# Kernel optimization log

Measured on AMD Instinct MI355X. Metric: run time of the kernel, lower is better.

Reference implementation:

```python
import jax, jax.numpy as jnp
import numpy as np

D_MODEL = 2048
N_HEADS = 16
D_HEAD = D_MODEL // N_HEADS


def setup_inputs() -> dict:
    key = jax.random.key(0)
    ks = jax.random.split(key, 8)
    B, T = 2, 2048
    s = 1.0 / np.sqrt(D_MODEL)
    return {
        "q": jax.random.normal(ks[0], (B, T, D_MODEL), jnp.float32),
        "k": jax.random.normal(ks[1], (B, T, D_MODEL), jnp.float32),
        "v": jax.random.normal(ks[2], (B, T, D_MODEL), jnp.float32),
        "Wq": jax.random.normal(ks[3], (D_MODEL, D_MODEL), jnp.float32) * s,
        "Wk": jax.random.normal(ks[4], (D_MODEL, D_MODEL), jnp.float32) * s,
        "Wv": jax.random.normal(ks[5], (D_MODEL, D_MODEL), jnp.float32) * s,
        "Wo": jax.random.normal(ks[6], (D_MODEL, D_MODEL), jnp.float32) * s,
        "bo": jax.random.normal(ks[7], (D_MODEL,), jnp.float32) * 0.01,
    }


def reference(q, k, v, Wq, Wk, Wv, Wo, bo):
    B, T, C = q.shape
    scale = D_HEAD ** -0.5
    # projections (torch Linear: x @ W.T), split into heads: [B, H, T, Dh]
    qh = (q @ Wq.T).reshape(B, T, N_HEADS, D_HEAD).transpose(0, 2, 1, 3)
    kh = (k @ Wk.T).reshape(B, -1, N_HEADS, D_HEAD).transpose(0, 2, 1, 3)
    vh = (v @ Wv.T).reshape(B, -1, N_HEADS, D_HEAD).transpose(0, 2, 1, 3)
    scores = jnp.einsum("bhqd,bhkd->bhqk", qh, kh) * scale  # [B,H,T,T]
    attn = jax.nn.softmax(scores, axis=-1)
    out = jnp.einsum("bhqk,bhkd->bhqd", attn, vh)  # [B,H,T,Dh]
    out = out.transpose(0, 2, 1, 3).reshape(B, T, C)
    return out @ Wo.T + bo
```

## Files before the change

### kernel.cpp

```cpp
#include <hip/hip_runtime.h>
#include <hip/hip_bf16.h>

typedef unsigned int u32;
typedef unsigned long long u64;
typedef unsigned short u16;
typedef __bf16 bf16_t;
typedef bf16_t bf16x8 __attribute__((ext_vector_type(8)));
typedef float f32x4 __attribute__((ext_vector_type(4)));
typedef float f32x4v __attribute__((ext_vector_type(4)));
typedef u16 u16x8 __attribute__((ext_vector_type(8)));

#define GLB __attribute__((address_space(1)))
#define LDSAS __attribute__((address_space(3)))

#define DM 2048
#define NH 16
#define DH 128
#define BB 2
#define TT 2048
#define MT (BB*TT)

static __device__ __forceinline__ u16 f2bf(float f){
    u32 x = __builtin_bit_cast(u32, f);
    return (u16)((x + 0x7FFFu + ((x >> 16) & 1u)) >> 16);
}

static __device__ __forceinline__ f32x4 mfma16(bf16x8 a, bf16x8 b, f32x4 c){
    return __builtin_amdgcn_mfma_f32_16x16x32_bf16(a, b, c, 0, 0, 0);
}

static __device__ __forceinline__ void gload_lds16(const u16* g, u16* l){
    __builtin_amdgcn_global_load_lds((const GLB u32*)g, (LDSAS u32*)l, 16, 0, 0);
}

__global__ __launch_bounds__(256) void cast_all(
    const float* __restrict__ q, const float* __restrict__ kin, const float* __restrict__ v,
    const float* __restrict__ wq, const float* __restrict__ wk, const float* __restrict__ wv,
    const float* __restrict__ wo,
    u16* __restrict__ qb, u16* __restrict__ kb, u16* __restrict__ vb,
    u16* __restrict__ wqb, u16* __restrict__ wkb, u16* __restrict__ wvb, u16* __restrict__ wob)
{
    const int QC = MT*DM/8;
    const int WC = DM*DM/8;
    int idx = blockIdx.x*256 + threadIdx.x;
    const float* src; u16* dst; int off;
    if (idx < 3*QC){
        int w = idx / QC; off = idx - w*QC;
        src = (w==0) ? q : (w==1) ? kin : v;
        dst = (w==0) ? qb : (w==1) ? kb : vb;
    } else {
        int j = idx - 3*QC; int w = j / WC; off = j - w*WC;
        src = (w==0) ? wq : (w==1) ? wk : (w==2) ? wv : wo;
        dst = (w==0) ? wqb : (w==1) ? wkb : (w==2) ? wvb : wob;
    }
    const f32x4v* s4 = (const f32x4v*)(src + (u64)off*8);
    f32x4v a = s4[0], b = s4[1];
    u16x8 r;
    r[0]=f2bf(a[0]); r[1]=f2bf(a[1]); r[2]=f2bf(a[2]); r[3]=f2bf(a[3]);
    r[4]=f2bf(b[0]); r[5]=f2bf(b[1]); r[6]=f2bf(b[2]); r[7]=f2bf(b[3]);
    *(u16x8*)(dst + (u64)off*8) = r;
}

template<int MODE>
__global__ __launch_bounds__(256) void gemm_bt(
    const u16* __restrict__ A0, const u16* __restrict__ B0, void* __restrict__ C0,
    const u16* __restrict__ A1, const u16* __restrict__ B1, void* __restrict__ C1,
    const u16* __restrict__ A2, const u16* __restrict__ B2, void* __restrict__ C2,
    const float* __restrict__ bias)
{
    __shared__ u16 Ash[128*32];
    __shared__ u16 Bsh[128*32];
    const u16 *A, *B; void* C;
    {
        int z = blockIdx.z;
        A = (z==0)?A0:(z==1)?A1:A2;
        B = (z==0)?B0:(z==1)?B1:B2;
        C = (z==0)?C0:(z==1)?C1:C2;
    }
    const int tid = threadIdx.x;
    const int lane = tid & 63;
    const int wave = tid >> 6;
    const int wr = wave >> 1, wc = wave & 1;
    const int g = lane >> 4, r16 = lane & 15;
    const int bm = blockIdx.y, bn = blockIdx.x;

    int srow[2], scol[2];
    #pragma unroll
    for (int rd = 0; rd < 2; rd++){
        int i = rd*256 + tid;
        int row = i >> 2;
        int c = (i & 3) ^ ((row >> 1) & 3);
        srow[rd] = row; scol[rd] = c*8;
    }
    const u16* Ag = A + (u64)(bm*128)*DM;
    const u16* Bg = B + (u64)(bn*128)*DM;

    int aoff[4], boff[4];
    #pragma unroll
    for (int mi = 0; mi < 4; mi++){
        int row = wr*64 + mi*16 + r16;
        int c = g ^ ((row >> 1) & 3);
        aoff[mi] = row*32 + c*8;
    }
    #pragma unroll
    for (int ni = 0; ni < 4; ni++){
        int row = wc*64 + ni*16 + r16;
        int c = g ^ ((row >> 1) & 3);
        boff[ni] = row*32 + c*8;
    }

    f32x4 acc[4][4] = {};

    for (int k0 = 0; k0 < DM; k0 += 32){
        #pragma unroll
        for (int rd = 0; rd < 2; rd++){
            int i = rd*256 + tid;
            gload_lds16(Ag + (u64)srow[rd]*DM + k0 + scol[rd], Ash + i*8);
            gload_lds16(Bg + (u64)srow[rd]*DM + k0 + scol[rd], Bsh + i*8);
        }
        __syncthreads();
        bf16x8 af[4], bfr[4];
        #pragma unroll
        for (int mi = 0; mi < 4; mi++) af[mi] = *(const bf16x8*)(Ash + aoff[mi]);
        #pragma unroll
        for (int ni = 0; ni < 4; ni++) bfr[ni] = *(const bf16x8*)(Bsh + boff[ni]);
        #pragma unroll
        for (int mi = 0; mi < 4; mi++)
            #pragma unroll
            for (int ni = 0; ni < 4; ni++)
                acc[mi][ni] = mfma16(af[mi], bfr[ni], acc[mi][ni]);
        __syncthreads();
    }

    #pragma unroll
    for (int mi = 0; mi < 4; mi++){
        #pragma unroll
        for (int ni = 0; ni < 4; ni++){
            int row0 = bm*128 + wr*64 + mi*16 + 4*g;
            int col  = bn*128 + wc*64 + ni*16 + r16;
            if (MODE == 0){
                u16* Cp = (u16*)C;
                #pragma unroll
                for (int rr = 0; rr < 4; rr++)
                    Cp[(u64)(row0+rr)*DM + col] = f2bf(acc[mi][ni][rr]);
            } else {
                float* Cp = (float*)C;
                float bv = bias[col];
                #pragma unroll
                for (int rr = 0; rr < 4; rr++)
                    Cp[(u64)(row0+rr)*DM + col] = acc[mi][ni][rr] + bv;
            }
        }
    }
}

__global__ __launch_bounds__(256) void transpose_v(
    const u16* __restrict__ Vh, u16* __restrict__ Vt)
{
    __shared__ u16 tile[64*80];
    int t0 = blockIdx.x*64, d0 = blockIdx.y*64, bh = blockIdx.z;
    int b = bh >> 4, h = bh & 15;
    int tid = threadIdx.x;
    #pragma unroll
    for (int rd = 0; rd < 2; rd++){
        int i = rd*256 + tid;
        int row = i >> 3, c = i & 7;
        u16x8 vv = *(const u16x8*)(Vh + (u64)(b*TT + t0 + row)*DM + h*DH + d0 + c*8);
        *(u16x8*)(tile + row*80 + c*8) = vv;
    }
    __syncthreads();
    #pragma unroll
    for (int rd = 0; rd < 2; rd++){
        int i = rd*256 + tid;
        int d = i >> 3, tc = (i & 7)*8;
        u16x8 vv;
        #pragma unroll
        for (int j = 0; j < 8; j++) vv[j] = tile[(tc + j)*80 + d];
        *(u16x8*)(Vt + (u64)(bh*DH + d0 + d)*TT + t0 + tc) = vv;
    }
}

__global__ __launch_bounds__(256) void flash_attn(
    const u16* __restrict__ Qh, const u16* __restrict__ Kh,
    const u16* __restrict__ Vt, u16* __restrict__ Ao)
{
    __shared__ u16 Ksh[64*128];
    __shared__ u16 Vsh[128*64];
    __shared__ u16 Psh[4*16*64];
    const int qt = blockIdx.x, h = blockIdx.y, b = blockIdx.z;
    const int tid = threadIdx.x, lane = tid & 63, wave = tid >> 6;
    const int g = lane >> 4, r16 = lane & 15;
    const int bh = b*NH + h;

    bf16x8 qf[4];
    {
        const u16* qp = Qh + (u64)(b*TT + qt*64 + wave*16 + r16)*DM + h*DH + g*8;
        #pragma unroll
        for (int kc = 0; kc < 4; kc++) qf[kc] = *(const bf16x8*)(qp + kc*32);
    }
    f32x4 accO[8] = {};
    float mrow[4], lrow[4];
    #pragma unroll
    for (int r = 0; r < 4; r++){ mrow[r] = -1e30f; lrow[r] = 0.f; }
    const float scale = 0.08838834764831845f;

    u16* Pw = Psh + wave*16*64;

    for (int kv0 = 0; kv0 < TT; kv0 += 64){
        #pragma unroll
        for (int rd = 0; rd < 4; rd++){
            int i = rd*256 + tid;
            int row = i >> 4, c = (i & 15) ^ (row & 7);
            gload_lds16(Kh + (u64)(b*TT + kv0 + row)*DM + h*DH + c*8, Ksh + i*8);
        }
        #pragma unroll
        for (int rd = 0; rd < 4; rd++){
            int i = rd*256 + tid;
            int row = i >> 3, c = (i & 7) ^ (row & 7);
            gload_lds16(Vt + (u64)(bh*DH + row)*TT + kv0 + c*8, Vsh + i*8);
        }
        __syncthreads();

        f32x4 s[4];
        #pragma unroll
        for (int nf = 0; nf < 4; nf++){
            f32x4 a = {0.f, 0.f, 0.f, 0.f};
            #pragma unroll
            for (int kc = 0; kc < 4; kc++){
                int row = nf*16 + r16;
                int c = (kc*4 + g) ^ (r16 & 7);
                bf16x8 kfr = *(const bf16x8*)(Ksh + row*128 + c*8);
                a = mfma16(qf[kc], kfr, a);
            }
            s[nf] = a * scale;
        }
        #pragma unroll
        for (int r = 0; r < 4; r++){
            float mx = fmaxf(fmaxf(s[0][r], s[1][r]), fmaxf(s[2][r], s[3][r]));
            #pragma unroll
            for (int d = 1; d < 16; d <<= 1) mx = fmaxf(mx, __shfl_xor(mx, d));
            float mnew = fmaxf(mrow[r], mx);
            float alpha = __expf(mrow[r] - mnew);
            mrow[r] = mnew;
            float ls = 0.f;
            #pragma unroll
            for (int nf = 0; nf < 4; nf++){
                float p = __expf(s[nf][r] - mnew);
                s[nf][r] = p;
                ls += p;
            }
            #pragma unroll
            for (int d = 1; d < 16; d <<= 1) ls += __shfl_xor(ls, d);
            lrow[r] = lrow[r]*alpha + ls;
            #pragma unroll
            for (int nfd = 0; nfd < 8; nfd++) accO[nfd][r] *= alpha;
        }
        #pragma unroll
        for (int r = 0; r < 4; r++){
            int qrow = 4*g + r;
            #pragma unroll
            for (int nf = 0; nf < 4; nf++){
                int kv = nf*16 + r16;
                int c = (kv >> 3) ^ (qrow & 7);
                Pw[qrow*64 + c*8 + (kv & 7)] = f2bf(s[nf][r]);
            }
        }
        #pragma unroll
        for (int kvc = 0; kvc < 2; kvc++){
            int cpa = (kvc*4 + g) ^ (r16 & 7);
            bf16x8 pa = *(const bf16x8*)(Pw + r16*64 + cpa*8);
            #pragma unroll
            for (int nfd = 0; nfd < 8; nfd++){
                int rowv = nfd*16 + r16;
                int cv = (kvc*4 + g) ^ (r16 & 7);
                bf16x8 vfr = *(const bf16x8*)(Vsh + rowv*64 + cv*8);
                accO[nfd] = mfma16(pa, vfr, accO[nfd]);
            }
        }
        __syncthreads();
    }

    #pragma unroll
    for (int nfd = 0; nfd < 8; nfd++){
        #pragma unroll
        for (int r = 0; r < 4; r++){
            int row = b*TT + qt*64 + wave*16 + 4*g + r;
            int col = h*DH + nfd*16 + r16;
            float o = accO[nfd][r] / lrow[r];
            Ao[(u64)row*DM + col] = f2bf(o);
        }
    }
}

extern "C" void kernel_launch(void* const* d_in, const int* in_sizes, int n_in,
                              void* d_out, int out_size, void* d_ws, size_t ws_size,
                              hipStream_t stream)
{
    const float* q  = (const float*)d_in[0];
    const float* k  = (const float*)d_in[1];
    const float* v  = (const float*)d_in[2];
    const float* wq = (const float*)d_in[3];
    const float* wk = (const float*)d_in[4];
    const float* wv = (const float*)d_in[5];
    const float* wo = (const float*)d_in[6];
    const float* bo = (const float*)d_in[7];
    float* out = (float*)d_out;

    const u64 SZQ = (u64)MT*DM;
    const u64 SZW = (u64)DM*DM;
    u16* ws  = (u16*)d_ws;
    u16* qb  = ws;
    u16* kb  = ws + SZQ;
    u16* vb  = ws + 2*SZQ;
    u16* wqb = ws + 3*SZQ;
    u16* wkb = wqb + SZW;
    u16* wvb = wqb + 2*SZW;
    u16* wob = wqb + 3*SZW;
    u16* qh  = ws + 5*SZQ;
    u16* kh  = ws + 6*SZQ;
    u16* vh  = ws + 7*SZQ;
    u16* vt  = qb;
    u16* ao  = vb;

    cast_all<<<dim3(20480), dim3(256), 0, stream>>>(
        q, k, v, wq, wk, wv, wo, qb, kb, vb, wqb, wkb, wvb, wob);

    gemm_bt<0><<<dim3(16, 32, 3), dim3(256), 0, stream>>>(
        qb, wqb, qh, kb, wkb, kh, vb, wvb, vh, nullptr);

    transpose_v<<<dim3(32, 2, 32), dim3(256), 0, stream>>>(vh, vt);

    flash_attn<<<dim3(32, 16, 2), dim3(256), 0, stream>>>(qh, kh, vt, ao);

    gemm_bt<1><<<dim3(16, 32, 1), dim3(256), 0, stream>>>(
        ao, wob, (void*)out, ao, wob, (void*)out, ao, wob, (void*)out, bo);
}
```

Baseline: 536.4 us.

## Rewrite flash attention with 32x32 MFMA, transposed S, double-buffered KV, register P

Replaces the flash attention kernel with a 512-thread, 256-query-row block that computes S transposed using 32x32x16 bf16 MFMA. Each lane then owns one query row, so softmax needs only a single cross-half shuffle. P is packed to bf16 in registers with v_cvt_pk and permlane32_swap instead of going through LDS. K/V tiles are double-buffered so the next tile's loads overlap compute, and blocks are remapped so heads sharing a query tile run close together. The aim is fewer LDS round trips and reductions and higher MFMA density, at the cost of more registers and inline asm that depends on the gfx950 ISA.

```diff
diff --git a/kernel.cpp b/kernel.cpp
--- a/kernel.cpp
+++ b/kernel.cpp
@@ -7,8 +7,10 @@
 typedef __bf16 bf16_t;
 typedef bf16_t bf16x8 __attribute__((ext_vector_type(8)));
 typedef float f32x4 __attribute__((ext_vector_type(4)));
+typedef float f32x16 __attribute__((ext_vector_type(16)));
 typedef float f32x4v __attribute__((ext_vector_type(4)));
 typedef u16 u16x8 __attribute__((ext_vector_type(8)));
+typedef u32 u32x4 __attribute__((ext_vector_type(4)));
 
 #define GLB __attribute__((address_space(1)))
 #define LDSAS __attribute__((address_space(3)))
@@ -27,6 +29,14 @@
 
 static __device__ __forceinline__ f32x4 mfma16(bf16x8 a, bf16x8 b, f32x4 c){
     return __builtin_amdgcn_mfma_f32_16x16x32_bf16(a, b, c, 0, 0, 0);
+}
+
+static __device__ __forceinline__ f32x16 mfma32(bf16x8 a, bf16x8 b, f32x16 c){
+    return __builtin_amdgcn_mfma_f32_32x32x16_bf16(a, b, c, 0, 0, 0);
+}
+
+static __device__ __forceinline__ u32 cvtpk(float lo, float hi){
+    u32 r; asm("v_cvt_pk_bf16_f32 %0, %1, %2" : "=v"(r) : "v"(lo), "v"(hi)); return r;
 }
 
 static __device__ __forceinline__ void gload_lds16(const u16* g, u16* l){
@@ -180,114 +190,137 @@
     }
 }
 
-__global__ __launch_bounds__(256) void flash_attn(
+static __device__ __forceinline__ void stage_kv(
+    const u16* __restrict__ Kbase, const u16* __restrict__ Vbase,
+    u16* ksh, u16* vsh, int tid)
+{
+    #pragma unroll
+    for (int rd = 0; rd < 2; rd++){
+        int ci = rd*512 + tid;
+        int row = ci >> 4, ch = (ci & 15) ^ (row & 7);
+        gload_lds16(Kbase + (u64)row*DM + ch*8, ksh + ci*8);
+    }
+    #pragma unroll
+    for (int rd = 0; rd < 2; rd++){
+        int ci = rd*512 + tid;
+        int row = ci >> 3, ch = (ci & 7) ^ (row & 7);
+        gload_lds16(Vbase + (u64)row*TT + ch*8, vsh + ci*8);
+    }
+}
+
+__global__ __launch_bounds__(512, 2) void flash_attn2(
     const u16* __restrict__ Qh, const u16* __restrict__ Kh,
     const u16* __restrict__ Vt, u16* __restrict__ Ao)
 {
-    __shared__ u16 Ksh[64*128];
-    __shared__ u16 Vsh[128*64];
-    __shared__ u16 Psh[4*16*64];
-    const int qt = blockIdx.x, h = blockIdx.y, b = blockIdx.z;
+    __shared__ __align__(16) u16 Ksh[2][64*128];
+    __shared__ __align__(16) u16 Vsh[2][128*64];
+    __shared__ __align__(16) float asc[8][32];
+
+    const int f = blockIdx.x + 8*(blockIdx.y + 16*blockIdx.z);
+    const int qt = f >> 5, bhl = f & 31;
+    const int b = bhl >> 4, h = bhl & 15;
+    const int bh = b*NH + h;
+
     const int tid = threadIdx.x, lane = tid & 63, wave = tid >> 6;
-    const int g = lane >> 4, r16 = lane & 15;
-    const int bh = b*NH + h;
-
-    bf16x8 qf[4];
+    const int l31 = lane & 31, hi = lane >> 5, l7 = lane & 7;
+    const float scale = 0.08838834764831845f;
+
+    bf16x8 qf[8];
     {
-        const u16* qp = Qh + (u64)(b*TT + qt*64 + wave*16 + r16)*DM + h*DH + g*8;
-        #pragma unroll
-        for (int kc = 0; kc < 4; kc++) qf[kc] = *(const bf16x8*)(qp + kc*32);
-    }
-    f32x4 accO[8] = {};
-    float mrow[4], lrow[4];
-    #pragma unroll
-    for (int r = 0; r < 4; r++){ mrow[r] = -1e30f; lrow[r] = 0.f; }
-    const float scale = 0.08838834764831845f;
-
-    u16* Pw = Psh + wave*16*64;
-
-    for (int kv0 = 0; kv0 < TT; kv0 += 64){
-        #pragma unroll
-        for (int rd = 0; rd < 4; rd++){
-            int i = rd*256 + tid;
-            int row = i >> 4, c = (i & 15) ^ (row & 7);
-            gload_lds16(Kh + (u64)(b*TT + kv0 + row)*DM + h*DH + c*8, Ksh + i*8);
-        }
-        #pragma unroll
-        for (int rd = 0; rd < 4; rd++){
-            int i = rd*256 + tid;
-            int row = i >> 3, c = (i & 7) ^ (row & 7);
-            gload_lds16(Vt + (u64)(bh*DH + row)*TT + kv0 + c*8, Vsh + i*8);
+        const u16* qp = Qh + (u64)(b*TT + qt*256 + wave*32 + l31)*DM + h*DH + hi*8;
+        #pragma unroll
+        for (int c = 0; c < 8; c++) qf[c] = *(const bf16x8*)(qp + c*16);
+    }
+
+    const u16* Kb = Kh + (u64)(b*TT)*DM + h*DH;
+    const u16* Vb = Vt + (u64)bh*DH*TT;
+
+    f32x16 accO[4] = {};
+    float m_ = -1e30f, l_ = 0.f;
+
+    stage_kv(Kb, Vb, Ksh[0], Vsh[0], tid);
+    __syncthreads();
+
+    for (int it = 0; it < TT/64; it++){
+        const int cur = it & 1;
+        if (it < TT/64 - 1)
+            stage_kv(Kb + (u64)(it+1)*64*DM, Vb + (it+1)*64,
+                     Ksh[cur^1], Vsh[cur^1], tid);
+
+        f32x16 s0 = {}, s1 = {};
+        #pragma unroll
+        for (int c = 0; c < 8; c++){
+            int ch = (2*c + hi) ^ l7;
+            bf16x8 k0 = *(const bf16x8*)(Ksh[cur] + l31*128 + ch*8);
+            bf16x8 k1 = *(const bf16x8*)(Ksh[cur] + (32 + l31)*128 + ch*8);
+            s0 = mfma32(k0, qf[c], s0);
+            s1 = mfma32(k1, qf[c], s1);
+        }
+
+        float pe[32];
+        #pragma unroll
+        for (int r = 0; r < 16; r++){ pe[r] = s0[r]*scale; pe[16+r] = s1[r]*scale; }
+        float mx = pe[0];
+        #pragma unroll
+        for (int i = 1; i < 32; i++) mx = fmaxf(mx, pe[i]);
+        mx = fmaxf(mx, __shfl_xor(mx, 32));
+        float mnew = fmaxf(m_, mx);
+        float alpha = __expf(m_ - mnew);
+        m_ = mnew;
+        float ls = 0.f;
+        #pragma unroll
+        for (int i = 0; i < 32; i++){ pe[i] = __expf(pe[i] - mnew); ls += pe[i]; }
+        ls += __shfl_xor(ls, 32);
+        l_ = l_*alpha + ls;
+
+        if (lane < 32) asc[wave][l31] = alpha;
+        f32x4 av[4];
+        #pragma unroll
+        for (int j = 0; j < 4; j++) av[j] = *(const f32x4*)&asc[wave][8*j + 4*hi];
+        #pragma unroll
+        for (int dt = 0; dt < 4; dt++)
+            #pragma unroll
+            for (int r = 0; r < 16; r++)
+                accO[dt][r] *= av[r>>2][r&3];
+
+        bf16x8 pa[4];
+        #pragma unroll
+        for (int c = 0; c < 4; c++){
+            u32 a0 = cvtpk(pe[8*c+0], pe[8*c+1]);
+            u32 b0 = cvtpk(pe[8*c+4], pe[8*c+5]);
+            u32 a1 = cvtpk(pe[8*c+2], pe[8*c+3]);
+            u32 b1 = cvtpk(pe[8*c+6], pe[8*c+7]);
+            asm volatile("v_permlane32_swap_b32 %0, %1" : "+v"(a0), "+v"(b0));
+            asm volatile("v_permlane32_swap_b32 %0, %1" : "+v"(a1), "+v"(b1));
+            u32x4 w = {a0, a1, b0, b1};
+            pa[c] = __builtin_bit_cast(bf16x8, w);
+        }
+
+        #pragma unroll
+        for (int dt = 0; dt < 4; dt++){
+            #pragma unroll
+            for (int c = 0; c < 4; c++){
+                int ch = (2*c + hi) ^ l7;
+                bf16x8 vf = *(const bf16x8*)(Vsh[cur] + (32*dt + l31)*64 + ch*8);
+                accO[dt] = mfma32(pa[c], vf, accO[dt]);
+            }
         }
         __syncthreads();
-
-        f32x4 s[4];
-        #pragma unroll
-        for (int nf = 0; nf < 4; nf++){
-            f32x4 a = {0.f, 0.f, 0.f, 0.f};
-            #pragma unroll
-            for (int kc = 0; kc < 4; kc++){
-                int row = nf*16 + r16;
-                int c = (kc*4 + g) ^ (r16 & 7);
-                bf16x8 kfr = *(const bf16x8*)(Ksh + row*128 + c*8);
-                a = mfma16(qf[kc], kfr, a);
-            }
-            s[nf] = a * scale;
-        }
-        #pragma unroll
-        for (int r = 0; r < 4; r++){
-            float mx = fmaxf(fmaxf(s[0][r], s[1][r]), fmaxf(s[2][r], s[3][r]));
-            #pragma unroll
-            for (int d = 1; d < 16; d <<= 1) mx = fmaxf(mx, __shfl_xor(mx, d));
-            float mnew = fmaxf(mrow[r], mx);
-            float alpha = __expf(mrow[r] - mnew);
-            mrow[r] = mnew;
-            float ls = 0.f;
-            #pragma unroll
-            for (int nf = 0; nf < 4; nf++){
-                float p = __expf(s[nf][r] - mnew);
-                s[nf][r] = p;
-                ls += p;
-            }
-            #pragma unroll
-            for (int d = 1; d < 16; d <<= 1) ls += __shfl_xor(ls, d);
-            lrow[r] = lrow[r]*alpha + ls;
-            #pragma unroll
-            for (int nfd = 0; nfd < 8; nfd++) accO[nfd][r] *= alpha;
-        }
-        #pragma unroll
-        for (int r = 0; r < 4; r++){
-            int qrow = 4*g + r;
-            #pragma unroll
-            for (int nf = 0; nf < 4; nf++){
-                int kv = nf*16 + r16;
-                int c = (kv >> 3) ^ (qrow & 7);
-                Pw[qrow*64 + c*8 + (kv & 7)] = f2bf(s[nf][r]);
-            }
-        }
-        #pragma unroll
-        for (int kvc = 0; kvc < 2; kvc++){
-            int cpa = (kvc*4 + g) ^ (r16 & 7);
-            bf16x8 pa = *(const bf16x8*)(Pw + r16*64 + cpa*8);
-            #pragma unroll
-            for (int nfd = 0; nfd < 8; nfd++){
-                int rowv = nfd*16 + r16;
-                int cv = (kvc*4 + g) ^ (r16 & 7);
-                bf16x8 vfr = *(const bf16x8*)(Vsh + rowv*64 + cv*8);
-                accO[nfd] = mfma16(pa, vfr, accO[nfd]);
-            }
-        }
-        __syncthreads();
-    }
-
-    #pragma unroll
-    for (int nfd = 0; nfd < 8; nfd++){
-        #pragma unroll
-        for (int r = 0; r < 4; r++){
-            int row = b*TT + qt*64 + wave*16 + 4*g + r;
-            int col = h*DH + nfd*16 + r16;
-            float o = accO[nfd][r] / lrow[r];
-            Ao[(u64)row*DM + col] = f2bf(o);
+    }
+
+    float linv = 1.f / l_;
+    if (lane < 32) asc[wave][l31] = linv;
+    f32x4 lv[4];
+    #pragma unroll
+    for (int j = 0; j < 4; j++) lv[j] = *(const f32x4*)&asc[wave][8*j + 4*hi];
+    #pragma unroll
+    for (int dt = 0; dt < 4; dt++){
+        #pragma unroll
+        for (int r = 0; r < 16; r++){
+            int qrow = (r&3) + 8*(r>>2) + 4*hi;
+            int grow = b*TT + qt*256 + wave*32 + qrow;
+            int gcol = h*DH + 32*dt + l31;
+            Ao[(u64)grow*DM + gcol] = f2bf(accO[dt][r] * lv[r>>2][r&3]);
         }
     }
 }
@@ -330,7 +363,7 @@
 
     transpose_v<<<dim3(32, 2, 32), dim3(256), 0, stream>>>(vh, vt);
 
-    flash_attn<<<dim3(32, 16, 2), dim3(256), 0, stream>>>(qh, kh, vt, ao);
+    flash_attn2<<<dim3(8, 16, 2), dim3(512), 0, stream>>>(qh, kh, vt, ao);
 
     gemm_bt<1><<<dim3(16, 32, 1), dim3(256), 0, stream>>>(
         ao, wob, (void*)out, ao, wob, (void*)out, ao, wob, (void*)out, bo);
```

Result: faster. 441.7 us (-17.7%).
